# Kernel tuning notes

Measured on AMD Instinct MI355X. Metric: run time of the kernel, lower is better.

## Reference

```python
import jax, jax.numpy as jnp
import numpy as np

NUM_HEADS = 16
D_MODEL = 1024
D_KV = 64
NUM_BUCKETS = 32
MAX_DISTANCE = 128


def _relative_position_bucket(relative_position, num_buckets=NUM_BUCKETS, max_distance=MAX_DISTANCE):
    # faithful port of the torch static method (bidirectional variant)
    n = -relative_position
    nb = num_buckets // 2
    ret = (n < 0).astype(jnp.int32) * nb
    n = jnp.abs(n)
    max_exact = nb // 2
    is_small = n < max_exact
    # guard log(0); is_small branch covers n < max_exact anyway
    val_if_large = max_exact + (
        jnp.log(jnp.maximum(n, 1).astype(jnp.float32) / max_exact)
        / np.log(max_distance / max_exact)
        * (nb - max_exact)
    ).astype(jnp.int32)
    val_if_large = jnp.minimum(val_if_large, nb - 1)
    return ret + jnp.where(is_small, n, val_if_large)


def _compute_bias(seq_len, rel_bias):
    ctx = jnp.arange(seq_len)[:, None]
    mem = jnp.arange(seq_len)[None, :]
    bucket = _relative_position_bucket(mem - ctx)  # [S, S]
    values = rel_bias[bucket]                      # [S, S, H]
    return jnp.transpose(values, (2, 0, 1))[None]  # [1, H, S, S]


def setup_inputs() -> dict:
    key = jax.random.key(0)
    ks = jax.random.split(key, 6)
    B, S = 4, 1024
    scale = 1.0 / np.sqrt(D_MODEL)
    return {
        "hidden_states": jax.random.normal(ks[0], (B, S, D_MODEL), jnp.float32),
        "attention_mask": jnp.ones((B, 1, 1, S), jnp.int32),
        "Wq": jax.random.normal(ks[1], (NUM_HEADS * D_KV, D_MODEL), jnp.float32) * scale,
        "Wk": jax.random.normal(ks[2], (NUM_HEADS * D_KV, D_MODEL), jnp.float32) * scale,
        "Wv": jax.random.normal(ks[3], (NUM_HEADS * D_KV, D_MODEL), jnp.float32) * scale,
        "Wo": jax.random.normal(ks[4], (D_MODEL, NUM_HEADS * D_KV), jnp.float32) * scale,
        "rel_bias": jax.random.normal(ks[5], (NUM_BUCKETS, NUM_HEADS), jnp.float32),
    }


def reference(hidden_states, attention_mask, Wq, Wk, Wv, Wo, rel_bias):
    B, S, _ = hidden_states.shape
    # projections (Linear with bias=False: x @ W.T), reshape to [B, S, H, d_kv]
    q = jnp.einsum('bsd,ed->bse', hidden_states, Wq).reshape(B, S, NUM_HEADS, D_KV)
    k = jnp.einsum('bsd,ed->bse', hidden_states, Wk).reshape(B, S, NUM_HEADS, D_KV)
    v = jnp.einsum('bsd,ed->bse', hidden_states, Wv).reshape(B, S, NUM_HEADS, D_KV)
    scores = jnp.einsum('bqhd,bkhd->bhqk', q, k) / np.sqrt(D_KV)
    scores = scores + _compute_bias(S, rel_bias)
    scores = jnp.where(attention_mask == 0, jnp.float32(-1e9), scores)
    attn_weights = jax.nn.softmax(scores, axis=-1)  # dropout is identity at eval
    attn_output = jnp.einsum('bhqk,bkhd->bqhd', attn_weights, v).reshape(B, S, NUM_HEADS * D_KV)
    output = jnp.einsum('bse,de->bsd', attn_output, Wo)
    return output, attn_weights
```

## Files before the change

kernel.cpp:

```cpp
#include <hip/hip_runtime.h>
#include <hip/hip_bf16.h>

#define BB 4
#define SS 1024
#define HH 16
#define DK 64
#define DM 1024
#define MM (BB * SS)

typedef __attribute__((ext_vector_type(8))) short bh8_t;
typedef __attribute__((ext_vector_type(4))) float f4_t;

#define MFMA(a, b, c) __builtin_amdgcn_mfma_f32_16x16x32_bf16(a, b, c, 0, 0, 0)

__device__ __forceinline__ short f2bf(float f) {
    unsigned u = __builtin_bit_cast(unsigned, f);
    u = (u + 0x7FFFu + ((u >> 16) & 1u)) >> 16;
    return (short)u;
}
__device__ __forceinline__ float bf2f(short h) {
    unsigned u = ((unsigned)(unsigned short)h) << 16;
    return __builtin_bit_cast(float, u);
}

__device__ __forceinline__ int rel_bucket(int rel) {
    int n = -rel;
    int ret = 0;
    if (n < 0) { ret = 16; n = -n; }
    int v;
    if (n < 8) {
        v = n;
    } else {
        float t = logf((float)n * 0.125f) / 2.7725887298583984f * 8.0f;
        v = 8 + (int)t;
        if (v > 15) v = 15;
    }
    return ret + v;
}

__global__ __launch_bounds__(256)
void k_proj_qk(const float* __restrict__ X, const float* __restrict__ Wq,
               const float* __restrict__ Wk,
               short* __restrict__ Qh, short* __restrict__ Ql,
               short* __restrict__ Kh, short* __restrict__ Kl) {
    const int z = blockIdx.z;
    const float* W = z ? Wk : Wq;
    short* Oh = z ? Kh : Qh;
    short* Ol = z ? Kl : Ql;

    __shared__ short Ah[128][40], Al[128][40], Bh[128][40], Bl[128][40];

    const int tid = threadIdx.x;
    const int m0 = blockIdx.y * 128, n0 = blockIdx.x * 128;
    const int wave = tid >> 6, lane = tid & 63;
    const int quad = lane >> 4, lm = lane & 15;
    const int wm = (wave >> 1) * 64, wn = (wave & 1) * 64;
    const int r = tid >> 1, sg = (tid & 1) * 16;

    f4_t acc[4][4];
#pragma unroll
    for (int i = 0; i < 4; ++i)
#pragma unroll
        for (int j = 0; j < 4; ++j) acc[i][j] = (f4_t){0.f, 0.f, 0.f, 0.f};

    for (int k0 = 0; k0 < DM; k0 += 32) {
        f4_t xa[4], wb[4];
#pragma unroll
        for (int u = 0; u < 4; ++u) {
            xa[u] = *(const f4_t*)(X + (size_t)(m0 + r) * DM + k0 + sg + u * 4);
            wb[u] = *(const f4_t*)(W + (size_t)(n0 + r) * DM + k0 + sg + u * 4);
        }
        __syncthreads();
#pragma unroll
        for (int u = 0; u < 4; ++u) {
            short4 hh, ll;
            hh.x = f2bf(xa[u][0]); ll.x = f2bf(xa[u][0] - bf2f(hh.x));
            hh.y = f2bf(xa[u][1]); ll.y = f2bf(xa[u][1] - bf2f(hh.y));
            hh.z = f2bf(xa[u][2]); ll.z = f2bf(xa[u][2] - bf2f(hh.z));
            hh.w = f2bf(xa[u][3]); ll.w = f2bf(xa[u][3] - bf2f(hh.w));
            *(short4*)&Ah[r][sg + u * 4] = hh;
            *(short4*)&Al[r][sg + u * 4] = ll;
            hh.x = f2bf(wb[u][0]); ll.x = f2bf(wb[u][0] - bf2f(hh.x));
            hh.y = f2bf(wb[u][1]); ll.y = f2bf(wb[u][1] - bf2f(hh.y));
            hh.z = f2bf(wb[u][2]); ll.z = f2bf(wb[u][2] - bf2f(hh.z));
            hh.w = f2bf(wb[u][3]); ll.w = f2bf(wb[u][3] - bf2f(hh.w));
            *(short4*)&Bh[r][sg + u * 4] = hh;
            *(short4*)&Bl[r][sg + u * 4] = ll;
        }
        __syncthreads();

        bh8_t ah[4], al[4];
#pragma unroll
        for (int i = 0; i < 4; ++i) {
            ah[i] = *(const bh8_t*)&Ah[wm + i * 16 + lm][quad * 8];
            al[i] = *(const bh8_t*)&Al[wm + i * 16 + lm][quad * 8];
        }
#pragma unroll
        for (int j = 0; j < 4; ++j) {
            bh8_t bhj = *(const bh8_t*)&Bh[wn + j * 16 + lm][quad * 8];
            bh8_t blj = *(const bh8_t*)&Bl[wn + j * 16 + lm][quad * 8];
#pragma unroll
            for (int i = 0; i < 4; ++i) {
                acc[i][j] = MFMA(al[i], bhj, acc[i][j]);
                acc[i][j] = MFMA(ah[i], blj, acc[i][j]);
                acc[i][j] = MFMA(ah[i], bhj, acc[i][j]);
            }
        }
    }

#pragma unroll
    for (int i = 0; i < 4; ++i)
#pragma unroll
        for (int j = 0; j < 4; ++j)
#pragma unroll
            for (int g = 0; g < 4; ++g) {
                const int row = m0 + wm + i * 16 + quad * 4 + g;
                const int col = n0 + wn + j * 16 + lm;
                const int b = row >> 10, s = row & 1023;
                const int hd = col >> 6, dk = col & 63;
                const float v = acc[i][j][g];
                const short vh = f2bf(v);
                const short vl = f2bf(v - bf2f(vh));
                const size_t o = ((size_t)((b * HH + hd) * SS + s)) * DK + dk;
                Oh[o] = vh;
                Ol[o] = vl;
            }
}

__global__ __launch_bounds__(256)
void k_proj_v(const float* __restrict__ X, const float* __restrict__ Wv,
              short* __restrict__ Vt) {
    __shared__ short As[128][40], Bs[128][40];

    const int tid = threadIdx.x;
    const int m0 = blockIdx.y * 128, n0 = blockIdx.x * 128;
    const int wave = tid >> 6, lane = tid & 63;
    const int quad = lane >> 4, lm = lane & 15;
    const int wm = (wave >> 1) * 64, wn = (wave & 1) * 64;
    const int r = tid >> 1, sg = (tid & 1) * 16;

    f4_t acc[4][4];
#pragma unroll
    for (int i = 0; i < 4; ++i)
#pragma unroll
        for (int j = 0; j < 4; ++j) acc[i][j] = (f4_t){0.f, 0.f, 0.f, 0.f};

    for (int k0 = 0; k0 < DM; k0 += 32) {
        f4_t xa[4], wb[4];
#pragma unroll
        for (int u = 0; u < 4; ++u) {
            xa[u] = *(const f4_t*)(X + (size_t)(m0 + r) * DM + k0 + sg + u * 4);
            wb[u] = *(const f4_t*)(Wv + (size_t)(n0 + r) * DM + k0 + sg + u * 4);
        }
        __syncthreads();
#pragma unroll
        for (int u = 0; u < 4; ++u) {
            short4 hh;
            hh.x = f2bf(xa[u][0]); hh.y = f2bf(xa[u][1]);
            hh.z = f2bf(xa[u][2]); hh.w = f2bf(xa[u][3]);
            *(short4*)&As[r][sg + u * 4] = hh;
            hh.x = f2bf(wb[u][0]); hh.y = f2bf(wb[u][1]);
            hh.z = f2bf(wb[u][2]); hh.w = f2bf(wb[u][3]);
            *(short4*)&Bs[r][sg + u * 4] = hh;
        }
        __syncthreads();

        bh8_t ah[4];
#pragma unroll
        for (int i = 0; i < 4; ++i)
            ah[i] = *(const bh8_t*)&As[wm + i * 16 + lm][quad * 8];
#pragma unroll
        for (int j = 0; j < 4; ++j) {
            bh8_t bhj = *(const bh8_t*)&Bs[wn + j * 16 + lm][quad * 8];
#pragma unroll
            for (int i = 0; i < 4; ++i) acc[i][j] = MFMA(ah[i], bhj, acc[i][j]);
        }
    }

#pragma unroll
    for (int i = 0; i < 4; ++i)
#pragma unroll
        for (int j = 0; j < 4; ++j)
#pragma unroll
            for (int g = 0; g < 4; ++g) {
                const int row = m0 + wm + i * 16 + quad * 4 + g;
                const int col = n0 + wn + j * 16 + lm;
                const int b = row >> 10, s = row & 1023;
                const int hd = col >> 6, dk = col & 63;
                Vt[((size_t)((b * HH + hd) * DK + dk)) * SS + s] = f2bf(acc[i][j][g]);
            }
}

__global__ __launch_bounds__(256)
void k_scores(const short* __restrict__ Qh, const short* __restrict__ Ql,
              const short* __restrict__ Kh, const short* __restrict__ Kl,
              const int* __restrict__ mask, const float* __restrict__ rb,
              float* __restrict__ P) {
    __shared__ short Qhs[128][72], Qls[128][72], Khs[128][72], Kls[128][72];
    __shared__ float biasS[256];
    __shared__ int maskS[128];

    const int bh = blockIdx.z, b = bh >> 4, hd = bh & 15;
    const int q0 = blockIdx.y * 128, k0 = blockIdx.x * 128;
    const int tid = threadIdx.x;
    const int wave = tid >> 6, lane = tid & 63;
    const int quad = lane >> 4, lm = lane & 15;
    const int wm = (wave >> 1) * 64, wn = (wave & 1) * 64;

    {
        const int r = tid >> 1, sg = (tid & 1) * 32;
        const size_t qo = ((size_t)bh * SS + q0 + r) * DK + sg;
        const size_t ko = ((size_t)bh * SS + k0 + r) * DK + sg;
#pragma unroll
        for (int u = 0; u < 4; ++u) {
            *(uint4*)&Qhs[r][sg + u * 8] = *(const uint4*)(Qh + qo + u * 8);
            *(uint4*)&Qls[r][sg + u * 8] = *(const uint4*)(Ql + qo + u * 8);
            *(uint4*)&Khs[r][sg + u * 8] = *(const uint4*)(Kh + ko + u * 8);
            *(uint4*)&Kls[r][sg + u * 8] = *(const uint4*)(Kl + ko + u * 8);
        }
    }
    if (tid < 255) biasS[tid] = rb[rel_bucket(k0 - q0 + tid - 127) * HH + hd];
    if (tid < 128) maskS[tid] = mask[b * SS + k0 + tid];
    __syncthreads();

    f4_t acc[4][4];
#pragma unroll
    for (int i = 0; i < 4; ++i)
#pragma unroll
        for (int j = 0; j < 4; ++j) acc[i][j] = (f4_t){0.f, 0.f, 0.f, 0.f};

#pragma unroll
    for (int ks = 0; ks < 2; ++ks) {
        bh8_t ah[4], al[4];
#pragma unroll
        for (int i = 0; i < 4; ++i) {
            ah[i] = *(const bh8_t*)&Qhs[wm + i * 16 + lm][ks * 32 + quad * 8];
            al[i] = *(const bh8_t*)&Qls[wm + i * 16 + lm][ks * 32 + quad * 8];
        }
#pragma unroll
        for (int j = 0; j < 4; ++j) {
            bh8_t bhj = *(const bh8_t*)&Khs[wn + j * 16 + lm][ks * 32 + quad * 8];
            bh8_t blj = *(const bh8_t*)&Kls[wn + j * 16 + lm][ks * 32 + quad * 8];
#pragma unroll
            for (int i = 0; i < 4; ++i) {
                acc[i][j] = MFMA(al[i], bhj, acc[i][j]);
                acc[i][j] = MFMA(ah[i], blj, acc[i][j]);
                acc[i][j] = MFMA(ah[i], bhj, acc[i][j]);
            }
        }
    }

#pragma unroll
    for (int i = 0; i < 4; ++i)
#pragma unroll
        for (int j = 0; j < 4; ++j)
#pragma unroll
            for (int g = 0; g < 4; ++g) {
                const int rowl = wm + i * 16 + quad * 4 + g;
                const int coll = wn + j * 16 + lm;
                float s = acc[i][j][g] * 0.125f + biasS[coll - rowl + 127];
                s = (maskS[coll] == 0) ? -1e9f : s;
                P[((size_t)bh * SS + q0 + rowl) * SS + k0 + coll] = s;
            }
}

__global__ __launch_bounds__(256)
void k_softmax(float* __restrict__ P) {
    const size_t row = blockIdx.x;
    float4* p = reinterpret_cast<float4*>(P + row * 1024);
    const int tid = threadIdx.x;
    float4 v = p[tid];

    float m = fmaxf(fmaxf(v.x, v.y), fmaxf(v.z, v.w));
#pragma unroll
    for (int off = 32; off > 0; off >>= 1) m = fmaxf(m, __shfl_xor(m, off, 64));

    __shared__ float redm[4], reds[4];
    const int wave = tid >> 6, lane = tid & 63;
    if (lane == 0) redm[wave] = m;
    __syncthreads();
    m = fmaxf(fmaxf(redm[0], redm[1]), fmaxf(redm[2], redm[3]));

    const float e0 = expf(v.x - m), e1 = expf(v.y - m);
    const float e2 = expf(v.z - m), e3 = expf(v.w - m);
    float ssum = e0 + e1 + e2 + e3;
#pragma unroll
    for (int off = 32; off > 0; off >>= 1) ssum += __shfl_xor(ssum, off, 64);
    if (lane == 0) reds[wave] = ssum;
    __syncthreads();
    ssum = reds[0] + reds[1] + reds[2] + reds[3];

    const float inv = 1.0f / ssum;
    p[tid] = make_float4(e0 * inv, e1 * inv, e2 * inv, e3 * inv);
}

__global__ __launch_bounds__(256)
void k_pv(const float* __restrict__ P, const short* __restrict__ Vt,
          short* __restrict__ AO) {
    __shared__ short As[128][40];
    __shared__ short Bs[64][40];

    const int bh = blockIdx.y, b = bh >> 4, hd = bh & 15;
    const int q0 = blockIdx.x * 128;
    const int tid = threadIdx.x;
    const int wave = tid >> 6, lane = tid & 63;
    const int quad = lane >> 4, lm = lane & 15;
    const int wm = wave * 32;
    const int rA = tid >> 1, sgA = (tid & 1) * 16;
    const int rB = tid >> 2, sgB = (tid & 3) * 8;

    f4_t acc[2][4];
#pragma unroll
    for (int i = 0; i < 2; ++i)
#pragma unroll
        for (int j = 0; j < 4; ++j) acc[i][j] = (f4_t){0.f, 0.f, 0.f, 0.f};

    for (int k0 = 0; k0 < SS; k0 += 32) {
        f4_t pr[4];
#pragma unroll
        for (int u = 0; u < 4; ++u)
            pr[u] = *(const f4_t*)(P + ((size_t)bh * SS + q0 + rA) * SS + k0 + sgA + u * 4);
        uint4 vb = *(const uint4*)(Vt + ((size_t)bh * DK + rB) * SS + k0 + sgB);
        __syncthreads();
#pragma unroll
        for (int u = 0; u < 4; ++u) {
            short4 hh;
            hh.x = f2bf(pr[u][0]); hh.y = f2bf(pr[u][1]);
            hh.z = f2bf(pr[u][2]); hh.w = f2bf(pr[u][3]);
            *(short4*)&As[rA][sgA + u * 4] = hh;
        }
        *(uint4*)&Bs[rB][sgB] = vb;
        __syncthreads();

        bh8_t af0 = *(const bh8_t*)&As[wm + lm][quad * 8];
        bh8_t af1 = *(const bh8_t*)&As[wm + 16 + lm][quad * 8];
#pragma unroll
        for (int j = 0; j < 4; ++j) {
            bh8_t bf = *(const bh8_t*)&Bs[j * 16 + lm][quad * 8];
            acc[0][j] = MFMA(af0, bf, acc[0][j]);
            acc[1][j] = MFMA(af1, bf, acc[1][j]);
        }
    }

#pragma unroll
    for (int i = 0; i < 2; ++i)
#pragma unroll
        for (int j = 0; j < 4; ++j)
#pragma unroll
            for (int g = 0; g < 4; ++g) {
                const int s = q0 + wm + i * 16 + quad * 4 + g;
                const int dk = j * 16 + lm;
                AO[((size_t)(b * SS + s)) * DM + hd * DK + dk] = f2bf(acc[i][j][g]);
            }
}

__global__ __launch_bounds__(256)
void k_out(const short* __restrict__ A, const float* __restrict__ Wo,
           float* __restrict__ Out) {
    __shared__ short As[128][40], Bs[128][40];

    const int tid = threadIdx.x;
    const int m0 = blockIdx.y * 128, n0 = blockIdx.x * 128;
    const int wave = tid >> 6, lane = tid & 63;
    const int quad = lane >> 4, lm = lane & 15;
    const int wm = (wave >> 1) * 64, wn = (wave & 1) * 64;
    const int r = tid >> 1, sg = (tid & 1) * 16;

    f4_t acc[4][4];
#pragma unroll
    for (int i = 0; i < 4; ++i)
#pragma unroll
        for (int j = 0; j < 4; ++j) acc[i][j] = (f4_t){0.f, 0.f, 0.f, 0.f};

    for (int k0 = 0; k0 < DM; k0 += 32) {
        uint4 a0 = *(const uint4*)(A + (size_t)(m0 + r) * DM + k0 + sg);
        uint4 a1 = *(const uint4*)(A + (size_t)(m0 + r) * DM + k0 + sg + 8);
        f4_t wb[4];
#pragma unroll
        for (int u = 0; u < 4; ++u)
            wb[u] = *(const f4_t*)(Wo + (size_t)(n0 + r) * DM + k0 + sg + u * 4);
        __syncthreads();
        *(uint4*)&As[r][sg] = a0;
        *(uint4*)&As[r][sg + 8] = a1;
#pragma unroll
        for (int u = 0; u < 4; ++u) {
            short4 hh;
            hh.x = f2bf(wb[u][0]); hh.y = f2bf(wb[u][1]);
            hh.z = f2bf(wb[u][2]); hh.w = f2bf(wb[u][3]);
            *(short4*)&Bs[r][sg + u * 4] = hh;
        }
        __syncthreads();

        bh8_t ah[4];
#pragma unroll
        for (int i = 0; i < 4; ++i)
            ah[i] = *(const bh8_t*)&As[wm + i * 16 + lm][quad * 8];
#pragma unroll
        for (int j = 0; j < 4; ++j) {
            bh8_t bhj = *(const bh8_t*)&Bs[wn + j * 16 + lm][quad * 8];
#pragma unroll
            for (int i = 0; i < 4; ++i) acc[i][j] = MFMA(ah[i], bhj, acc[i][j]);
        }
    }

#pragma unroll
    for (int i = 0; i < 4; ++i)
#pragma unroll
        for (int j = 0; j < 4; ++j)
#pragma unroll
            for (int g = 0; g < 4; ++g)
                Out[(size_t)(m0 + wm + i * 16 + quad * 4 + g) * DM + n0 + wn + j * 16 + lm] =
                    acc[i][j][g];
}

extern "C" void kernel_launch(void* const* d_in, const int* in_sizes, int n_in,
                              void* d_out, int out_size, void* d_ws, size_t ws_size,
                              hipStream_t stream) {
    const float* X    = (const float*)d_in[0];
    const int*   mask = (const int*)d_in[1];
    const float* Wq   = (const float*)d_in[2];
    const float* Wk   = (const float*)d_in[3];
    const float* Wv   = (const float*)d_in[4];
    const float* Wo   = (const float*)d_in[5];
    const float* rb   = (const float*)d_in[6];

    float* out = (float*)d_out;
    float* P   = out + (size_t)BB * SS * DM;

    short* ws = (short*)d_ws;
    short* Qh = ws;
    short* Ql = ws + (size_t)4194304;
    short* Kh = ws + (size_t)8388608;
    short* Kl = ws + (size_t)12582912;
    short* Vt = ws + (size_t)16777216;
    short* AO = ws;

    k_proj_qk<<<dim3(8, 32, 2), 256, 0, stream>>>(X, Wq, Wk, Qh, Ql, Kh, Kl);
    k_proj_v <<<dim3(8, 32, 1), 256, 0, stream>>>(X, Wv, Vt);
    k_scores <<<dim3(8, 8, BB * HH), 256, 0, stream>>>(Qh, Ql, Kh, Kl, mask, rb, P);
    k_softmax<<<dim3(BB * HH * SS), 256, 0, stream>>>(P);
    k_pv     <<<dim3(8, BB * HH), 256, 0, stream>>>(P, Vt, AO);
    k_out    <<<dim3(8, 32), 256, 0, stream>>>(AO, Wo, out);
}
```

Baseline: 654.9 us.

## Fuse scores, softmax and PV into one kernel over 16-row query blocks

Replaces the separate scores, softmax and PV kernels with one fused kernel. Each block handles 16 query rows of one head, keeps the full score rows in LDS, computes the softmax there and writes P only once. It then does PV straight from LDS, using a cross-wave reduction in shared memory. This removes the extra global round trips of the 256 MB P matrix (write, read, write, read). The cost is about 75 KB of LDS per block, which limits occupancy, K and V reloads per 16-row block with no LDS staging, and a block-index swizzle.

```diff
diff --git a/kernel.cpp b/kernel.cpp
--- a/kernel.cpp
+++ b/kernel.cpp
@@ -191,167 +191,172 @@
             }
 }
 
+#define EPAD 1044
+
 __global__ __launch_bounds__(256)
-void k_scores(const short* __restrict__ Qh, const short* __restrict__ Ql,
-              const short* __restrict__ Kh, const short* __restrict__ Kl,
-              const int* __restrict__ mask, const float* __restrict__ rb,
-              float* __restrict__ P) {
-    __shared__ short Qhs[128][72], Qls[128][72], Khs[128][72], Kls[128][72];
-    __shared__ float biasS[256];
-    __shared__ int maskS[128];
-
-    const int bh = blockIdx.z, b = bh >> 4, hd = bh & 15;
-    const int q0 = blockIdx.y * 128, k0 = blockIdx.x * 128;
+void k_fused(const short* __restrict__ Qh, const short* __restrict__ Ql,
+             const short* __restrict__ Kh, const short* __restrict__ Kl,
+             const short* __restrict__ Vt, const int* __restrict__ mask,
+             const float* __restrict__ rb, float* __restrict__ P,
+             short* __restrict__ AO) {
+    __shared__ __align__(16) char smem[75328];
+    float* E     = (float*)smem;
+    float* redS  = (float*)smem;
+    float* biasS = (float*)(smem + 66816);
+    int*   maskS = (int*)(smem + 70976);
+    float* wmaxS = (float*)(smem + 75072);
+
     const int tid = threadIdx.x;
+    const int bid = blockIdx.x;
+    const int swz = (bid & 7) * 512 + (bid >> 3);
+    const int qb = swz & 63, bh = swz >> 6;
+    const int b = bh >> 4, hd = bh & 15;
+    const int q0 = qb * 16;
     const int wave = tid >> 6, lane = tid & 63;
     const int quad = lane >> 4, lm = lane & 15;
-    const int wm = (wave >> 1) * 64, wn = (wave & 1) * 64;
+
+    for (int i = tid; i < 1040; i += 256)
+        biasS[i] = rb[rel_bucket(i - q0 - 15) * HH + hd];
+    for (int i = tid; i < 1024; i += 256) maskS[i] = mask[b * SS + i];
+
+    bh8_t qah[2], qal[2];
+#pragma unroll
+    for (int ks = 0; ks < 2; ++ks) {
+        const size_t qo = ((size_t)bh * SS + q0 + lm) * DK + ks * 32 + quad * 8;
+        qah[ks] = *(const bh8_t*)(Qh + qo);
+        qal[ks] = *(const bh8_t*)(Ql + qo);
+    }
+    __syncthreads();
+
+    float pmax[4] = {-3.0e38f, -3.0e38f, -3.0e38f, -3.0e38f};
+
+    for (int kt = 0; kt < 8; ++kt) {
+        const int kb = kt * 128 + wave * 32;
+        f4_t acc[2];
+        acc[0] = (f4_t){0.f, 0.f, 0.f, 0.f};
+        acc[1] = (f4_t){0.f, 0.f, 0.f, 0.f};
+        bh8_t kh[2][2], kl[2][2];
+#pragma unroll
+        for (int j = 0; j < 2; ++j)
+#pragma unroll
+            for (int ks = 0; ks < 2; ++ks) {
+                const size_t ko =
+                    ((size_t)bh * SS + kb + j * 16 + lm) * DK + ks * 32 + quad * 8;
+                kh[j][ks] = *(const bh8_t*)(Kh + ko);
+                kl[j][ks] = *(const bh8_t*)(Kl + ko);
+            }
+#pragma unroll
+        for (int j = 0; j < 2; ++j)
+#pragma unroll
+            for (int ks = 0; ks < 2; ++ks) {
+                acc[j] = MFMA(qal[ks], kh[j][ks], acc[j]);
+                acc[j] = MFMA(qah[ks], kl[j][ks], acc[j]);
+                acc[j] = MFMA(qah[ks], kh[j][ks], acc[j]);
+            }
+#pragma unroll
+        for (int j = 0; j < 2; ++j) {
+            const int col = kb + j * 16 + lm;
+            const int msk = maskS[col];
+#pragma unroll
+            for (int g = 0; g < 4; ++g) {
+                const int rl = quad * 4 + g;
+                float s = acc[j][g] * 0.125f + biasS[col - rl + 15];
+                s = (msk == 0) ? -1e9f : s;
+                E[rl * EPAD + col] = s;
+                pmax[g] = fmaxf(pmax[g], s);
+            }
+        }
+    }
+#pragma unroll
+    for (int g = 0; g < 4; ++g) {
+        float m = pmax[g];
+        m = fmaxf(m, __shfl_xor(m, 1, 64));
+        m = fmaxf(m, __shfl_xor(m, 2, 64));
+        m = fmaxf(m, __shfl_xor(m, 4, 64));
+        m = fmaxf(m, __shfl_xor(m, 8, 64));
+        if (lm == 0) wmaxS[wave * 16 + quad * 4 + g] = m;
+    }
+    __syncthreads();
 
     {
-        const int r = tid >> 1, sg = (tid & 1) * 32;
-        const size_t qo = ((size_t)bh * SS + q0 + r) * DK + sg;
-        const size_t ko = ((size_t)bh * SS + k0 + r) * DK + sg;
-#pragma unroll
-        for (int u = 0; u < 4; ++u) {
-            *(uint4*)&Qhs[r][sg + u * 8] = *(const uint4*)(Qh + qo + u * 8);
-            *(uint4*)&Qls[r][sg + u * 8] = *(const uint4*)(Ql + qo + u * 8);
-            *(uint4*)&Khs[r][sg + u * 8] = *(const uint4*)(Kh + ko + u * 8);
-            *(uint4*)&Kls[r][sg + u * 8] = *(const uint4*)(Kl + ko + u * 8);
-        }
-    }
-    if (tid < 255) biasS[tid] = rb[rel_bucket(k0 - q0 + tid - 127) * HH + hd];
-    if (tid < 128) maskS[tid] = mask[b * SS + k0 + tid];
+        const int row = tid >> 4;
+        const int cc = (tid & 15) * 4;
+        const float m = fmaxf(fmaxf(wmaxS[row], wmaxS[16 + row]),
+                              fmaxf(wmaxS[32 + row], wmaxS[48 + row]));
+        f4_t ev[16];
+        float sum = 0.f;
+#pragma unroll
+        for (int u = 0; u < 16; ++u) {
+            f4_t s4 = *(const f4_t*)&E[row * EPAD + cc + u * 64];
+            f4_t e;
+            e[0] = expf(s4[0] - m);
+            e[1] = expf(s4[1] - m);
+            e[2] = expf(s4[2] - m);
+            e[3] = expf(s4[3] - m);
+            ev[u] = e;
+            sum += e[0] + e[1] + e[2] + e[3];
+        }
+        sum += __shfl_xor(sum, 1, 64);
+        sum += __shfl_xor(sum, 2, 64);
+        sum += __shfl_xor(sum, 4, 64);
+        sum += __shfl_xor(sum, 8, 64);
+        const float inv = 1.0f / sum;
+        float* Pr = P + ((size_t)bh * SS + q0 + row) * SS;
+#pragma unroll
+        for (int u = 0; u < 16; ++u) {
+            f4_t p;
+            p[0] = ev[u][0] * inv;
+            p[1] = ev[u][1] * inv;
+            p[2] = ev[u][2] * inv;
+            p[3] = ev[u][3] * inv;
+            *(f4_t*)&E[row * EPAD + cc + u * 64] = p;
+            *(f4_t*)(Pr + cc + u * 64) = p;
+        }
+    }
     __syncthreads();
 
-    f4_t acc[4][4];
-#pragma unroll
-    for (int i = 0; i < 4; ++i)
-#pragma unroll
-        for (int j = 0; j < 4; ++j) acc[i][j] = (f4_t){0.f, 0.f, 0.f, 0.f};
-
-#pragma unroll
-    for (int ks = 0; ks < 2; ++ks) {
-        bh8_t ah[4], al[4];
-#pragma unroll
-        for (int i = 0; i < 4; ++i) {
-            ah[i] = *(const bh8_t*)&Qhs[wm + i * 16 + lm][ks * 32 + quad * 8];
-            al[i] = *(const bh8_t*)&Qls[wm + i * 16 + lm][ks * 32 + quad * 8];
-        }
-#pragma unroll
-        for (int j = 0; j < 4; ++j) {
-            bh8_t bhj = *(const bh8_t*)&Khs[wn + j * 16 + lm][ks * 32 + quad * 8];
-            bh8_t blj = *(const bh8_t*)&Kls[wn + j * 16 + lm][ks * 32 + quad * 8];
-#pragma unroll
-            for (int i = 0; i < 4; ++i) {
-                acc[i][j] = MFMA(al[i], bhj, acc[i][j]);
-                acc[i][j] = MFMA(ah[i], blj, acc[i][j]);
-                acc[i][j] = MFMA(ah[i], bhj, acc[i][j]);
-            }
-        }
-    }
-
-#pragma unroll
-    for (int i = 0; i < 4; ++i)
-#pragma unroll
-        for (int j = 0; j < 4; ++j)
-#pragma unroll
-            for (int g = 0; g < 4; ++g) {
-                const int rowl = wm + i * 16 + quad * 4 + g;
-                const int coll = wn + j * 16 + lm;
-                float s = acc[i][j][g] * 0.125f + biasS[coll - rowl + 127];
-                s = (maskS[coll] == 0) ? -1e9f : s;
-                P[((size_t)bh * SS + q0 + rowl) * SS + k0 + coll] = s;
-            }
-}
-
-__global__ __launch_bounds__(256)
-void k_softmax(float* __restrict__ P) {
-    const size_t row = blockIdx.x;
-    float4* p = reinterpret_cast<float4*>(P + row * 1024);
-    const int tid = threadIdx.x;
-    float4 v = p[tid];
-
-    float m = fmaxf(fmaxf(v.x, v.y), fmaxf(v.z, v.w));
-#pragma unroll
-    for (int off = 32; off > 0; off >>= 1) m = fmaxf(m, __shfl_xor(m, off, 64));
-
-    __shared__ float redm[4], reds[4];
-    const int wave = tid >> 6, lane = tid & 63;
-    if (lane == 0) redm[wave] = m;
+    f4_t acc[4];
+#pragma unroll
+    for (int f = 0; f < 4; ++f) acc[f] = (f4_t){0.f, 0.f, 0.f, 0.f};
+
+    for (int kk = 0; kk < 8; ++kk) {
+        const int kg = wave * 256 + kk * 32 + quad * 8;
+        f4_t p0 = *(const f4_t*)&E[lm * EPAD + kg];
+        f4_t p1 = *(const f4_t*)&E[lm * EPAD + kg + 4];
+        bh8_t pa;
+        pa[0] = f2bf(p0[0]); pa[1] = f2bf(p0[1]);
+        pa[2] = f2bf(p0[2]); pa[3] = f2bf(p0[3]);
+        pa[4] = f2bf(p1[0]); pa[5] = f2bf(p1[1]);
+        pa[6] = f2bf(p1[2]); pa[7] = f2bf(p1[3]);
+#pragma unroll
+        for (int f = 0; f < 4; ++f) {
+            bh8_t vb =
+                *(const bh8_t*)(Vt + ((size_t)bh * DK + f * 16 + lm) * SS + kg);
+            acc[f] = MFMA(pa, vb, acc[f]);
+        }
+    }
     __syncthreads();
-    m = fmaxf(fmaxf(redm[0], redm[1]), fmaxf(redm[2], redm[3]));
-
-    const float e0 = expf(v.x - m), e1 = expf(v.y - m);
-    const float e2 = expf(v.z - m), e3 = expf(v.w - m);
-    float ssum = e0 + e1 + e2 + e3;
-#pragma unroll
-    for (int off = 32; off > 0; off >>= 1) ssum += __shfl_xor(ssum, off, 64);
-    if (lane == 0) reds[wave] = ssum;
+#pragma unroll
+    for (int f = 0; f < 4; ++f)
+#pragma unroll
+        for (int g = 0; g < 4; ++g)
+            redS[((size_t)wave * 16 + quad * 4 + g) * 64 + f * 16 + lm] = acc[f][g];
     __syncthreads();
-    ssum = reds[0] + reds[1] + reds[2] + reds[3];
-
-    const float inv = 1.0f / ssum;
-    p[tid] = make_float4(e0 * inv, e1 * inv, e2 * inv, e3 * inv);
-}
-
-__global__ __launch_bounds__(256)
-void k_pv(const float* __restrict__ P, const short* __restrict__ Vt,
-          short* __restrict__ AO) {
-    __shared__ short As[128][40];
-    __shared__ short Bs[64][40];
-
-    const int bh = blockIdx.y, b = bh >> 4, hd = bh & 15;
-    const int q0 = blockIdx.x * 128;
-    const int tid = threadIdx.x;
-    const int wave = tid >> 6, lane = tid & 63;
-    const int quad = lane >> 4, lm = lane & 15;
-    const int wm = wave * 32;
-    const int rA = tid >> 1, sgA = (tid & 1) * 16;
-    const int rB = tid >> 2, sgB = (tid & 3) * 8;
-
-    f4_t acc[2][4];
-#pragma unroll
-    for (int i = 0; i < 2; ++i)
-#pragma unroll
-        for (int j = 0; j < 4; ++j) acc[i][j] = (f4_t){0.f, 0.f, 0.f, 0.f};
-
-    for (int k0 = 0; k0 < SS; k0 += 32) {
-        f4_t pr[4];
-#pragma unroll
-        for (int u = 0; u < 4; ++u)
-            pr[u] = *(const f4_t*)(P + ((size_t)bh * SS + q0 + rA) * SS + k0 + sgA + u * 4);
-        uint4 vb = *(const uint4*)(Vt + ((size_t)bh * DK + rB) * SS + k0 + sgB);
-        __syncthreads();
-#pragma unroll
-        for (int u = 0; u < 4; ++u) {
-            short4 hh;
-            hh.x = f2bf(pr[u][0]); hh.y = f2bf(pr[u][1]);
-            hh.z = f2bf(pr[u][2]); hh.w = f2bf(pr[u][3]);
-            *(short4*)&As[rA][sgA + u * 4] = hh;
-        }
-        *(uint4*)&Bs[rB][sgB] = vb;
-        __syncthreads();
-
-        bh8_t af0 = *(const bh8_t*)&As[wm + lm][quad * 8];
-        bh8_t af1 = *(const bh8_t*)&As[wm + 16 + lm][quad * 8];
-#pragma unroll
-        for (int j = 0; j < 4; ++j) {
-            bh8_t bf = *(const bh8_t*)&Bs[j * 16 + lm][quad * 8];
-            acc[0][j] = MFMA(af0, bf, acc[0][j]);
-            acc[1][j] = MFMA(af1, bf, acc[1][j]);
-        }
-    }
-
-#pragma unroll
-    for (int i = 0; i < 2; ++i)
-#pragma unroll
-        for (int j = 0; j < 4; ++j)
-#pragma unroll
-            for (int g = 0; g < 4; ++g) {
-                const int s = q0 + wm + i * 16 + quad * 4 + g;
-                const int dk = j * 16 + lm;
-                AO[((size_t)(b * SS + s)) * DM + hd * DK + dk] = f2bf(acc[i][j][g]);
-            }
+
+    {
+        const int flat = tid * 4;
+        const int q = flat >> 6, dk = flat & 63;
+        f4_t s0 = *(const f4_t*)&redS[(0 * 16 + q) * 64 + dk];
+        f4_t s1 = *(const f4_t*)&redS[(1 * 16 + q) * 64 + dk];
+        f4_t s2 = *(const f4_t*)&redS[(2 * 16 + q) * 64 + dk];
+        f4_t s3 = *(const f4_t*)&redS[(3 * 16 + q) * 64 + dk];
+        short4 o;
+        o.x = f2bf(s0[0] + s1[0] + s2[0] + s3[0]);
+        o.y = f2bf(s0[1] + s1[1] + s2[1] + s3[1]);
+        o.z = f2bf(s0[2] + s1[2] + s2[2] + s3[2]);
+        o.w = f2bf(s0[3] + s1[3] + s2[3] + s3[3]);
+        *(short4*)(AO + ((size_t)(b * SS + q0 + q)) * DM + hd * DK + dk) = o;
+    }
 }
 
 __global__ __launch_bounds__(256)
@@ -433,12 +438,10 @@
     short* Kh = ws + (size_t)8388608;
     short* Kl = ws + (size_t)12582912;
     short* Vt = ws + (size_t)16777216;
-    short* AO = ws;
+    short* AO = ws + (size_t)20971520;
 
     k_proj_qk<<<dim3(8, 32, 2), 256, 0, stream>>>(X, Wq, Wk, Qh, Ql, Kh, Kl);
     k_proj_v <<<dim3(8, 32, 1), 256, 0, stream>>>(X, Wv, Vt);
-    k_scores <<<dim3(8, 8, BB * HH), 256, 0, stream>>>(Qh, Ql, Kh, Kl, mask, rb, P);
-    k_softmax<<<dim3(BB * HH * SS), 256, 0, stream>>>(P);
-    k_pv     <<<dim3(8, BB * HH), 256, 0, stream>>>(P, Vt, AO);
+    k_fused  <<<dim3(4096), 256, 0, stream>>>(Qh, Ql, Kh, Kl, Vt, mask, rb, P, AO);
     k_out    <<<dim3(8, 32), 256, 0, stream>>>(AO, Wo, out);
 }
```

After: 646.8 us. No clear change (-1.2%).
